# Optimization experiments

Measured on AMD Instinct MI355X. Metric: run time of the kernel, lower is better.

Reference implementation:

```python
import jax, jax.numpy as jnp
import numpy as np

N_NODES = 50000
N_EDGES = 1000000
IN_CH = 256
HID_CH = 128
HEADS = 2
OUT_CH = 3
NEG_SLOPE = 0.2  # PyG GATConv default leaky_relu slope


def setup_inputs() -> dict:
    key = jax.random.key(0)
    ks = jax.random.split(key, 10)
    s = 0.1
    x = jax.random.normal(ks[0], (N_NODES, IN_CH), dtype=jnp.float32)
    edge_index = jax.random.randint(ks[1], (2, N_EDGES), 0, N_NODES, dtype=jnp.int64)
    # GATConv layer 1 (heads=2, concat=True)
    W1 = jax.random.normal(ks[2], (IN_CH, HEADS * HID_CH), dtype=jnp.float32) * s
    a_src1 = jax.random.normal(ks[3], (HEADS, HID_CH), dtype=jnp.float32) * s
    a_dst1 = jax.random.normal(ks[4], (HEADS, HID_CH), dtype=jnp.float32) * s
    b1 = jnp.zeros((HEADS * HID_CH,), dtype=jnp.float32)
    # GATConv layer 2 (heads=1, concat=False)
    W2 = jax.random.normal(ks[5], (HEADS * HID_CH, OUT_CH), dtype=jnp.float32) * s
    a_src2 = jax.random.normal(ks[6], (1, OUT_CH), dtype=jnp.float32) * s
    a_dst2 = jax.random.normal(ks[7], (1, OUT_CH), dtype=jnp.float32) * s
    b2 = jnp.zeros((OUT_CH,), dtype=jnp.float32)
    return dict(x=x, edge_index=edge_index, W1=W1, a_src1=a_src1, a_dst1=a_dst1,
                b1=b1, W2=W2, a_src2=a_src2, a_dst2=a_dst2, b2=b2)


def gat_layer(x, edge_index, W, a_src, a_dst, b, concat):
    # x: [N, F_in]; W: [F_in, H*C]; a_src/a_dst: [H, C]
    n = x.shape[0]
    H, C = a_src.shape
    h = (x @ W).reshape(n, H, C)                       # [N, H, C]
    al_s = jnp.einsum('nhc,hc->nh', h, a_src)          # [N, H]
    al_d = jnp.einsum('nhc,hc->nh', h, a_dst)          # [N, H]
    src, dst = edge_index[0], edge_index[1]
    e = jax.nn.leaky_relu(al_s[src] + al_d[dst], NEG_SLOPE)   # [E, H]
    # segment softmax over incoming edges of each dst node
    e_max = jax.ops.segment_max(e, dst, num_segments=n)       # [N, H]
    w = jnp.exp(e - e_max[dst])                                # [E, H]
    denom = jax.ops.segment_sum(w, dst, num_segments=n)        # [N, H]
    alpha = w / jnp.maximum(denom[dst], 1e-16)                 # [E, H]
    out = jax.ops.segment_sum(h[src] * alpha[:, :, None], dst, num_segments=n)  # [N, H, C]
    out = out.reshape(n, H * C) if concat else out.mean(axis=1)
    return out + b


def reference(x, edge_index, W1, a_src1, a_dst1, b1, W2, a_src2, a_dst2, b2):
    # dropout(p=0.6) is identity in eval mode
    h = jax.nn.elu(gat_layer(x, edge_index, W1, a_src1, a_dst1, b1, concat=True))
    h = gat_layer(h, edge_index, W2, a_src2, a_dst2, b2, concat=False)
    return jax.nn.log_softmax(h, axis=1)
```

## Files before the change

kernel.cpp:

```cpp
#include <hip/hip_runtime.h>

#define N_NODES 50000
#define N_EDGES 1000000
#define FIN 256
#define F1  256
#define OUTC 3
#define SUBCAP 32
#define GEMM_BLOCKS ((N_NODES + 63) / 64)
#define EDGE_BLOCKS ((N_EDGES + 255) / 256)

typedef __attribute__((ext_vector_type(8))) short  short8;
typedef __attribute__((ext_vector_type(4))) float  f32x4;
typedef __attribute__((ext_vector_type(2))) float  f32x2;

__device__ __forceinline__ unsigned short f2bf(float f) {
  unsigned int x; __builtin_memcpy(&x, &f, 4);
  x += 0x7fffu + ((x >> 16) & 1u);
  return (unsigned short)(x >> 16);
}
__device__ __forceinline__ float u2f(unsigned int x) {
  float f; __builtin_memcpy(&f, &x, 4); return f;
}
__device__ __forceinline__ float wredmax(float v) {
  #pragma unroll
  for (int m = 32; m > 0; m >>= 1) v = fmaxf(v, __shfl_xor(v, m));
  return v;
}
__device__ __forceinline__ float wredsum(float v) {
  #pragma unroll
  for (int m = 32; m > 0; m >>= 1) v += __shfl_xor(v, m);
  return v;
}

__global__ __launch_bounds__(256) void k_t(const float* __restrict__ w1,
                                           unsigned short* __restrict__ w1t,
                                           int* __restrict__ deg2) {
  int idx = blockIdx.x * 256 + threadIdx.x;
  int k = idx >> 8, n = idx & 255;
  w1t[n * 256 + k] = f2bf(w1[k * 256 + n]);
  if (idx < 2 * N_NODES) deg2[idx] = 0;
  int i2 = idx + 65536;
  if (i2 < 2 * N_NODES) deg2[i2] = 0;
}

__global__ __launch_bounds__(256) void k_bg(
    const float* __restrict__ x,
    const unsigned short* __restrict__ w1t,
    const float* __restrict__ a_src1,
    const float* __restrict__ a_dst1,
    unsigned short* __restrict__ h1b,
    float* __restrict__ als1,
    float* __restrict__ ald1,
    const int* __restrict__ ei,
    int* __restrict__ deg2, unsigned short* __restrict__ bucket) {
  const int t = threadIdx.x;

  if (blockIdx.x >= GEMM_BLOCKS) {
    __shared__ int sflag;
    if (t < 64) {
      int idx = 2 * (t * 15625 + 7) + 1;
      unsigned long long b = __ballot(ei[idx] != 0);
      if (t == 0) sflag = (b != 0ull) ? 1 : 0;
    }
    __syncthreads();
    const int f = sflag;
    int e = (blockIdx.x - GEMM_BLOCKS) * 256 + t;
    if (e < N_EDGES) {
      int s, d;
      if (f) { s = ei[e];     d = ei[N_EDGES + e]; }
      else   { s = ei[2 * e]; d = ei[2 * (N_EDGES + e)]; }
      int sub = e & 1;
      int pos = atomicAdd(&deg2[d * 2 + sub], 1);
      if (pos < SUBCAP) bucket[d * 64 + sub * SUBCAP + pos] = (unsigned short)s;
    }
    return;
  }

  const int wv   = t >> 6;
  const int lane = t & 63;
  const int m    = lane & 15;
  const int quad = lane >> 4;
  const int row0 = blockIdx.x * 64 + wv * 16;

  int arow = row0 + m;
  if (arow > N_NODES - 1) arow = N_NODES - 1;
  const float* xrow = x + (size_t)arow * FIN + quad * 8;

  short8 af[8];
  #pragma unroll
  for (int kk = 0; kk < 8; ++kk) {
    f32x4 v0 = *(const f32x4*)(xrow + kk * 32);
    f32x4 v1 = *(const f32x4*)(xrow + kk * 32 + 4);
    short8 fr;
    #pragma unroll
    for (int j = 0; j < 4; ++j) {
      fr[j]     = (short)f2bf(v0[j]);
      fr[j + 4] = (short)f2bf(v1[j]);
    }
    af[kk] = fr;
  }

  f32x4 acc[16];
  #pragma unroll
  for (int c = 0; c < 16; ++c) {
    const unsigned short* bp = w1t + (size_t)(c * 16 + m) * FIN + quad * 8;
    f32x4 a = {0.f, 0.f, 0.f, 0.f};
    #pragma unroll
    for (int kk = 0; kk < 8; ++kk) {
      short8 bf = *(const short8*)(bp + kk * 32);
      a = __builtin_amdgcn_mfma_f32_16x16x32_bf16(af[kk], bf, a, 0, 0, 0);
    }
    acc[c] = a;
  }

  float s0[4] = {0,0,0,0}, s1[4] = {0,0,0,0}, d0[4] = {0,0,0,0}, d1[4] = {0,0,0,0};
  #pragma unroll
  for (int c = 0; c < 16; ++c) {
    int ch = c * 16 + m;
    float av = a_src1[ch];
    float dv = a_dst1[ch];
    if (c < 8) {
      #pragma unroll
      for (int r = 0; r < 4; ++r) { s0[r] += acc[c][r] * av; d0[r] += acc[c][r] * dv; }
    } else {
      #pragma unroll
      for (int r = 0; r < 4; ++r) { s1[r] += acc[c][r] * av; d1[r] += acc[c][r] * dv; }
    }
  }
  #pragma unroll
  for (int msk = 1; msk < 16; msk <<= 1) {
    #pragma unroll
    for (int r = 0; r < 4; ++r) {
      s0[r] += __shfl_xor(s0[r], msk);
      s1[r] += __shfl_xor(s1[r], msk);
      d0[r] += __shfl_xor(d0[r], msk);
      d1[r] += __shfl_xor(d1[r], msk);
    }
  }
  #pragma unroll
  for (int r = 0; r < 4; ++r) {
    int row = row0 + quad * 4 + r;
    if (row < N_NODES) {
      unsigned short* hrow = h1b + (size_t)row * F1 + m;
      #pragma unroll
      for (int c = 0; c < 16; ++c) hrow[c * 16] = f2bf(acc[c][r]);
      if (m == 0) {
        als1[row * 2 + 0] = s0[r]; als1[row * 2 + 1] = s1[r];
        ald1[row * 2 + 0] = d0[r]; ald1[row * 2 + 1] = d1[r];
      }
    }
  }
}

__global__ __launch_bounds__(256) void k_attn1(
    const unsigned short* __restrict__ bucket,
    const int* __restrict__ deg2,
    const float* __restrict__ als1,
    const float* __restrict__ ald1,
    const unsigned short* __restrict__ h1b,
    const float* __restrict__ b1,
    const float* __restrict__ w2,
    const float* __restrict__ a_src2,
    const float* __restrict__ a_dst2,
    float4* __restrict__ h2pack,
    float* __restrict__ ald2) {
  const int wv   = threadIdx.x >> 6;
  const int lane = threadIdx.x & 63;
  const int n = blockIdx.x * 4 + wv;
  if (n >= N_NODES) return;
  const int c0 = min(deg2[n * 2 + 0], SUBCAP);
  const int c1 = min(deg2[n * 2 + 1], SUBCAP);
  const int dg = c0 + c1;
  const float ad0  = ald1[n * 2 + 0];
  const float ad1v = ald1[n * 2 + 1];
  const float2* alsv = (const float2*)als1;

  const int l31   = lane & 31;
  const int ehalf = lane >> 5;
  const bool head1 = (l31 >= 16);

  float l0 = -1e30f, l1 = -1e30f; int sreg = 0;
  if (lane < dg) {
    int bidx = lane < c0 ? lane : (SUBCAP + lane - c0);
    sreg = (int)bucket[n * 64 + bidx];
    float2 a = alsv[sreg];
    l0 = a.x + ad0;  l0 = l0 > 0.f ? l0 : 0.2f * l0;
    l1 = a.y + ad1v; l1 = l1 > 0.f ? l1 : 0.2f * l1;
  }
  const float m0 = wredmax(l0), m1 = wredmax(l1);
  const float e0 = (lane < dg) ? __expf(l0 - m0) : 0.f;
  const float e1 = (lane < dg) ? __expf(l1 - m1) : 0.f;
  const float sum0 = wredsum(e0), sum1 = wredsum(e1);
  const float inv = 1.f / fmaxf(head1 ? sum1 : sum0, 1e-16f);

  f32x2 accv[4] = {{0.f,0.f},{0.f,0.f},{0.f,0.f},{0.f,0.f}};
  const int pairs = (dg + 1) >> 1;
  for (int e = 0; e < pairs; e += 8) {
    float w[8]; int sv[8];
    #pragma unroll
    for (int k = 0; k < 8; ++k) {
      int eidx = 2 * (e + k) + ehalf;
      int esel = eidx & 63;
      float w0 = __shfl(e0, esel);
      float w1 = __shfl(e1, esel);
      sv[k] = __shfl(sreg, esel);
      w[k] = head1 ? w1 : w0;
      if (eidx >= dg) w[k] = 0.f;
    }
    uint4 hv[8];
    #pragma unroll
    for (int k = 0; k < 8; ++k)
      hv[k] = *(const uint4*)(h1b + (size_t)sv[k] * F1 + l31 * 8);
    #pragma unroll
    for (int k = 0; k < 8; ++k) {
      const unsigned int* hu = (const unsigned int*)&hv[k];
      f32x2 wv2 = {w[k], w[k]};
      #pragma unroll
      for (int j = 0; j < 4; ++j) {
        unsigned int u = hu[j];
        f32x2 h;
        h.x = u2f(u << 16);
        h.y = u2f(u & 0xffff0000u);
        accv[j] = __builtin_elementwise_fma(wv2, h, accv[j]);
      }
    }
  }

  float* av = (float*)accv;
  #pragma unroll
  for (int j = 0; j < 8; ++j) av[j] += __shfl_xor(av[j], 32);

  float p0 = 0.f, p1 = 0.f, p2 = 0.f;
  #pragma unroll
  for (int j = 0; j < 8; ++j) {
    int ch = l31 * 8 + j;
    float tt = av[j] * inv + b1[ch];
    tt = tt > 0.f ? tt : __expf(tt) - 1.f;
    p0 = fmaf(tt, w2[ch * 3 + 0], p0);
    p1 = fmaf(tt, w2[ch * 3 + 1], p1);
    p2 = fmaf(tt, w2[ch * 3 + 2], p2);
  }
  p0 = wredsum(p0) * 0.5f;
  p1 = wredsum(p1) * 0.5f;
  p2 = wredsum(p2) * 0.5f;
  if (lane == 0) {
    float als2v = p0 * a_src2[0] + p1 * a_src2[1] + p2 * a_src2[2];
    h2pack[n] = make_float4(p0, p1, p2, als2v);
    ald2[n] = p0 * a_dst2[0] + p1 * a_dst2[1] + p2 * a_dst2[2];
  }
}

__global__ __launch_bounds__(256) void k_attn2(
    const unsigned short* __restrict__ bucket,
    const int* __restrict__ deg2,
    const float4* __restrict__ h2pack,
    const float* __restrict__ ald2,
    const float* __restrict__ b2,
    float* __restrict__ out) {
  const int wv   = threadIdx.x >> 6;
  const int lane = threadIdx.x & 63;
  const int n = blockIdx.x * 4 + wv;
  if (n >= N_NODES) return;
  const int c0 = min(deg2[n * 2 + 0], SUBCAP);
  const int c1 = min(deg2[n * 2 + 1], SUBCAP);
  const int dg = c0 + c1;
  const float adn = ald2[n];

  float l = -1e30f;
  float4 hp = make_float4(0.f, 0.f, 0.f, 0.f);
  if (lane < dg) {
    int bidx = lane < c0 ? lane : (SUBCAP + lane - c0);
    int s = (int)bucket[n * 64 + bidx];
    hp = h2pack[s];
    l = hp.w + adn;
    l = l > 0.f ? l : 0.2f * l;
  }
  const float m = wredmax(l);
  const float e = (lane < dg) ? __expf(l - m) : 0.f;
  const float sum = wredsum(e);
  const float inv = 1.f / fmaxf(sum, 1e-16f);
  float p0 = wredsum(e * hp.x);
  float p1 = wredsum(e * hp.y);
  float p2 = wredsum(e * hp.z);

  if (lane == 0) {
    float o0 = p0 * inv + b2[0];
    float o1 = p1 * inv + b2[1];
    float o2 = p2 * inv + b2[2];
    float mm = fmaxf(o0, fmaxf(o1, o2));
    float ls = logf(__expf(o0 - mm) + __expf(o1 - mm) + __expf(o2 - mm));
    out[n * 3 + 0] = o0 - mm - ls;
    out[n * 3 + 1] = o1 - mm - ls;
    out[n * 3 + 2] = o2 - mm - ls;
  }
}

extern "C" void kernel_launch(void* const* d_in, const int* in_sizes, int n_in,
                              void* d_out, int out_size, void* d_ws, size_t ws_size,
                              hipStream_t stream) {
  (void)in_sizes; (void)n_in; (void)out_size; (void)ws_size;
  const float* x      = (const float*)d_in[0];
  const int*   ei     = (const int*)d_in[1];
  const float* W1     = (const float*)d_in[2];
  const float* a_src1 = (const float*)d_in[3];
  const float* a_dst1 = (const float*)d_in[4];
  const float* b1     = (const float*)d_in[5];
  const float* W2     = (const float*)d_in[6];
  const float* a_src2 = (const float*)d_in[7];
  const float* a_dst2 = (const float*)d_in[8];
  const float* b2     = (const float*)d_in[9];
  float* out = (float*)d_out;

  char* p = (char*)d_ws;
  auto alloc = [&](size_t bytes) -> char* {
    char* r = p; p += (bytes + 511) & ~(size_t)511; return r;
  };
  unsigned short* w1t  = (unsigned short*)alloc(65536ull * 2);
  unsigned short* h1b  = (unsigned short*)alloc((size_t)N_NODES * F1 * 2);
  float*  als1   = (float*)alloc((size_t)N_NODES * 2 * 4);
  float*  ald1   = (float*)alloc((size_t)N_NODES * 2 * 4);
  float4* h2pack = (float4*)alloc((size_t)N_NODES * 16);
  float*  ald2   = (float*)alloc((size_t)N_NODES * 4);
  int*    deg2   = (int*)alloc((size_t)N_NODES * 2 * 4);
  unsigned short* bucket = (unsigned short*)alloc((size_t)N_NODES * 64 * 2);

  hipLaunchKernelGGL(k_t, dim3(256), dim3(256), 0, stream, W1, w1t, deg2);
  hipLaunchKernelGGL(k_bg, dim3(GEMM_BLOCKS + EDGE_BLOCKS), dim3(256), 0, stream,
                     x, w1t, a_src1, a_dst1, h1b, als1, ald1, ei, deg2, bucket);
  hipLaunchKernelGGL(k_attn1, dim3((N_NODES + 3) / 4), dim3(256), 0, stream,
                     bucket, deg2, als1, ald1, h1b, b1, W2, a_src2, a_dst2,
                     h2pack, ald2);
  hipLaunchKernelGGL(k_attn2, dim3((N_NODES + 3) / 4), dim3(256), 0, stream,
                     bucket, deg2, h2pack, ald2, b2, out);
}
```

Baseline: 262.2 us.

## Split layer-1 attention into alpha, channel-chunked aggregation, and post kernels

Replaces the fused per-node attention-and-gather kernel with three passes. The first computes softmax weights and packs each one, quantized to 16 bits, together with the 16-bit source index. The second aggregates 32-channel slices, with the chunk chosen by blockIdx&7, so each chunk's slice of h1 is a smaller working set that can stay cache-resident. The third applies bias, ELU and the layer-2 projection from an fp16 intermediate. This is meant to improve cache locality of the random row gathers. In exchange it adds extra global traffic for the pack and intermediate buffers, two more launches, narrower 64-byte gathers, and precision loss from quantizing alpha and storing the result in fp16.

```diff
diff --git a/kernel.cpp b/kernel.cpp
--- a/kernel.cpp
+++ b/kernel.cpp
@@ -8,10 +8,13 @@
 #define SUBCAP 32
 #define GEMM_BLOCKS ((N_NODES + 63) / 64)
 #define EDGE_BLOCKS ((N_EDGES + 255) / 256)
+#define NODE_BLOCKS ((N_NODES + 3) / 4)
+#define AGG_NB (N_NODES / 16)
 
 typedef __attribute__((ext_vector_type(8))) short  short8;
 typedef __attribute__((ext_vector_type(4))) float  f32x4;
 typedef __attribute__((ext_vector_type(2))) float  f32x2;
+typedef __attribute__((ext_vector_type(4))) _Float16 h16x4;
 
 __device__ __forceinline__ unsigned short f2bf(float f) {
   unsigned int x; __builtin_memcpy(&x, &f, 4);
@@ -152,12 +155,96 @@
   }
 }
 
-__global__ __launch_bounds__(256) void k_attn1(
+__global__ __launch_bounds__(256) void k_alpha(
     const unsigned short* __restrict__ bucket,
     const int* __restrict__ deg2,
     const float* __restrict__ als1,
     const float* __restrict__ ald1,
-    const unsigned short* __restrict__ h1b,
+    unsigned int* __restrict__ pack0,
+    unsigned int* __restrict__ pack1) {
+  const int wv   = threadIdx.x >> 6;
+  const int lane = threadIdx.x & 63;
+  const int n = blockIdx.x * 4 + wv;
+  if (n >= N_NODES) return;
+  const int c0 = min(deg2[n * 2 + 0], SUBCAP);
+  const int c1 = min(deg2[n * 2 + 1], SUBCAP);
+  const int dg = c0 + c1;
+  const float ad0  = ald1[n * 2 + 0];
+  const float ad1v = ald1[n * 2 + 1];
+  const float2* alsv = (const float2*)als1;
+
+  float l0 = -1e30f, l1 = -1e30f; int s = 0;
+  if (lane < dg) {
+    int bidx = lane < c0 ? lane : (SUBCAP + lane - c0);
+    s = (int)bucket[n * 64 + bidx];
+    float2 a = alsv[s];
+    l0 = a.x + ad0;  l0 = l0 > 0.f ? l0 : 0.2f * l0;
+    l1 = a.y + ad1v; l1 = l1 > 0.f ? l1 : 0.2f * l1;
+  }
+  const float m0 = wredmax(l0), m1 = wredmax(l1);
+  const float e0 = (lane < dg) ? __expf(l0 - m0) : 0.f;
+  const float e1 = (lane < dg) ? __expf(l1 - m1) : 0.f;
+  const float sum0 = wredsum(e0), sum1 = wredsum(e1);
+  unsigned int q0 = (unsigned int)rintf(e0 / fmaxf(sum0, 1e-16f) * 65535.f);
+  unsigned int q1 = (unsigned int)rintf(e1 / fmaxf(sum1, 1e-16f) * 65535.f);
+  unsigned int su = (unsigned int)s << 16;
+  pack0[n * 64 + lane] = su | q0;
+  pack1[n * 64 + lane] = su | q1;
+}
+
+__global__ __launch_bounds__(256) void k_agg(
+    const int* __restrict__ deg2,
+    const unsigned int* __restrict__ pack0,
+    const unsigned int* __restrict__ pack1,
+    const unsigned int* __restrict__ h1b32,
+    unsigned int* __restrict__ h2agg32) {
+  const int chunk = blockIdx.x & 7;
+  const int nb    = blockIdx.x >> 3;
+  const int g     = threadIdx.x >> 4;
+  const int l16   = threadIdx.x & 15;
+  const int n = nb * 16 + g;
+
+  const int c0 = min(deg2[n * 2 + 0], SUBCAP);
+  const int c1 = min(deg2[n * 2 + 1], SUBCAP);
+  const int dg = c0 + c1;
+
+  const unsigned int* pk = (chunk >= 4 ? pack1 : pack0) + (size_t)n * 64;
+  unsigned int r0 = __builtin_nontemporal_load(pk + l16);
+  unsigned int r1 = (dg > 16) ? __builtin_nontemporal_load(pk + 16 + l16) : 0u;
+  unsigned int r2 = (dg > 32) ? __builtin_nontemporal_load(pk + 32 + l16) : 0u;
+  unsigned int r3 = (dg > 48) ? __builtin_nontemporal_load(pk + 48 + l16) : 0u;
+
+  const unsigned int* slab = h1b32 + chunk * 16 + l16;
+  f32x2 acc = {0.f, 0.f};
+
+  #define AGG_ROUND(RQ, BASE)                                              \
+    if (BASE < dg) {                                                       \
+      _Pragma("unroll")                                                    \
+      for (int j = 0; j < 16; ++j) {                                       \
+        unsigned int rec = (unsigned int)__shfl((int)(RQ), j, 16);         \
+        float a = (float)(rec & 0xffffu) * (1.f / 65535.f);                \
+        unsigned int u = slab[(size_t)(rec >> 16) * 128];                  \
+        f32x2 h; h.x = u2f(u << 16); h.y = u2f(u & 0xffff0000u);           \
+        f32x2 av = {a, a};                                                 \
+        acc = __builtin_elementwise_fma(av, h, acc);                       \
+      }                                                                    \
+    }
+  AGG_ROUND(r0, 0)
+  AGG_ROUND(r1, 16)
+  AGG_ROUND(r2, 32)
+  AGG_ROUND(r3, 48)
+  #undef AGG_ROUND
+
+  _Float16 o0 = (_Float16)acc.x, o1 = (_Float16)acc.y;
+  unsigned short w0, w1;
+  __builtin_memcpy(&w0, &o0, 2);
+  __builtin_memcpy(&w1, &o1, 2);
+  unsigned int ow = (unsigned int)w0 | ((unsigned int)w1 << 16);
+  __builtin_nontemporal_store(ow, h2agg32 + (size_t)n * 128 + chunk * 16 + l16);
+}
+
+__global__ __launch_bounds__(256) void k_post(
+    const _Float16* __restrict__ h2agg,
     const float* __restrict__ b1,
     const float* __restrict__ w2,
     const float* __restrict__ a_src2,
@@ -168,81 +255,20 @@
   const int lane = threadIdx.x & 63;
   const int n = blockIdx.x * 4 + wv;
   if (n >= N_NODES) return;
-  const int c0 = min(deg2[n * 2 + 0], SUBCAP);
-  const int c1 = min(deg2[n * 2 + 1], SUBCAP);
-  const int dg = c0 + c1;
-  const float ad0  = ald1[n * 2 + 0];
-  const float ad1v = ald1[n * 2 + 1];
-  const float2* alsv = (const float2*)als1;
-
-  const int l31   = lane & 31;
-  const int ehalf = lane >> 5;
-  const bool head1 = (l31 >= 16);
-
-  float l0 = -1e30f, l1 = -1e30f; int sreg = 0;
-  if (lane < dg) {
-    int bidx = lane < c0 ? lane : (SUBCAP + lane - c0);
-    sreg = (int)bucket[n * 64 + bidx];
-    float2 a = alsv[sreg];
-    l0 = a.x + ad0;  l0 = l0 > 0.f ? l0 : 0.2f * l0;
-    l1 = a.y + ad1v; l1 = l1 > 0.f ? l1 : 0.2f * l1;
-  }
-  const float m0 = wredmax(l0), m1 = wredmax(l1);
-  const float e0 = (lane < dg) ? __expf(l0 - m0) : 0.f;
-  const float e1 = (lane < dg) ? __expf(l1 - m1) : 0.f;
-  const float sum0 = wredsum(e0), sum1 = wredsum(e1);
-  const float inv = 1.f / fmaxf(head1 ? sum1 : sum0, 1e-16f);
-
-  f32x2 accv[4] = {{0.f,0.f},{0.f,0.f},{0.f,0.f},{0.f,0.f}};
-  const int pairs = (dg + 1) >> 1;
-  for (int e = 0; e < pairs; e += 8) {
-    float w[8]; int sv[8];
-    #pragma unroll
-    for (int k = 0; k < 8; ++k) {
-      int eidx = 2 * (e + k) + ehalf;
-      int esel = eidx & 63;
-      float w0 = __shfl(e0, esel);
-      float w1 = __shfl(e1, esel);
-      sv[k] = __shfl(sreg, esel);
-      w[k] = head1 ? w1 : w0;
-      if (eidx >= dg) w[k] = 0.f;
-    }
-    uint4 hv[8];
-    #pragma unroll
-    for (int k = 0; k < 8; ++k)
-      hv[k] = *(const uint4*)(h1b + (size_t)sv[k] * F1 + l31 * 8);
-    #pragma unroll
-    for (int k = 0; k < 8; ++k) {
-      const unsigned int* hu = (const unsigned int*)&hv[k];
-      f32x2 wv2 = {w[k], w[k]};
-      #pragma unroll
-      for (int j = 0; j < 4; ++j) {
-        unsigned int u = hu[j];
-        f32x2 h;
-        h.x = u2f(u << 16);
-        h.y = u2f(u & 0xffff0000u);
-        accv[j] = __builtin_elementwise_fma(wv2, h, accv[j]);
-      }
-    }
-  }
-
-  float* av = (float*)accv;
-  #pragma unroll
-  for (int j = 0; j < 8; ++j) av[j] += __shfl_xor(av[j], 32);
-
+  h16x4 hv = *(const h16x4*)(h2agg + (size_t)n * F1 + lane * 4);
   float p0 = 0.f, p1 = 0.f, p2 = 0.f;
   #pragma unroll
-  for (int j = 0; j < 8; ++j) {
-    int ch = l31 * 8 + j;
-    float tt = av[j] * inv + b1[ch];
+  for (int j = 0; j < 4; ++j) {
+    int ch = lane * 4 + j;
+    float tt = (float)hv[j] + b1[ch];
     tt = tt > 0.f ? tt : __expf(tt) - 1.f;
     p0 = fmaf(tt, w2[ch * 3 + 0], p0);
     p1 = fmaf(tt, w2[ch * 3 + 1], p1);
     p2 = fmaf(tt, w2[ch * 3 + 2], p2);
   }
-  p0 = wredsum(p0) * 0.5f;
-  p1 = wredsum(p1) * 0.5f;
-  p2 = wredsum(p2) * 0.5f;
+  p0 = wredsum(p0);
+  p1 = wredsum(p1);
+  p2 = wredsum(p2);
   if (lane == 0) {
     float als2v = p0 * a_src2[0] + p1 * a_src2[1] + p2 * a_src2[2];
     h2pack[n] = make_float4(p0, p1, p2, als2v);
@@ -323,13 +349,19 @@
   float*  ald2   = (float*)alloc((size_t)N_NODES * 4);
   int*    deg2   = (int*)alloc((size_t)N_NODES * 2 * 4);
   unsigned short* bucket = (unsigned short*)alloc((size_t)N_NODES * 64 * 2);
+  unsigned int* pack0 = (unsigned int*)alloc((size_t)N_NODES * 64 * 4);
+  unsigned int* pack1 = (unsigned int*)alloc((size_t)N_NODES * 64 * 4);
+  unsigned int* h2agg32 = (unsigned int*)alloc((size_t)N_NODES * 128 * 4);
 
   hipLaunchKernelGGL(k_t, dim3(256), dim3(256), 0, stream, W1, w1t, deg2);
   hipLaunchKernelGGL(k_bg, dim3(GEMM_BLOCKS + EDGE_BLOCKS), dim3(256), 0, stream,
                      x, w1t, a_src1, a_dst1, h1b, als1, ald1, ei, deg2, bucket);
-  hipLaunchKernelGGL(k_attn1, dim3((N_NODES + 3) / 4), dim3(256), 0, stream,
-                     bucket, deg2, als1, ald1, h1b, b1, W2, a_src2, a_dst2,
-                     h2pack, ald2);
-  hipLaunchKernelGGL(k_attn2, dim3((N_NODES + 3) / 4), dim3(256), 0, stream,
+  hipLaunchKernelGGL(k_alpha, dim3(NODE_BLOCKS), dim3(256), 0, stream,
+                     bucket, deg2, als1, ald1, pack0, pack1);
+  hipLaunchKernelGGL(k_agg, dim3(8 * AGG_NB), dim3(256), 0, stream,
+                     deg2, pack0, pack1, (const unsigned int*)h1b, h2agg32);
+  hipLaunchKernelGGL(k_post, dim3(NODE_BLOCKS), dim3(256), 0, stream,
+                     (const _Float16*)h2agg32, b1, W2, a_src2, a_dst2, h2pack, ald2);
+  hipLaunchKernelGGL(k_attn2, dim3(NODE_BLOCKS), dim3(256), 0, stream,
                      bucket, deg2, h2pack, ald2, b2, out);
 }
```

Measured after the change: 302.9 us. 15.5% more time.
